# Kernel tuning notes

Measured on AMD Instinct MI355X. Metric: run time of the kernel, lower is better.

Reference implementation:

```python
import jax, jax.numpy as jnp
import numpy as np

T = 2048          # tokens (prefill, single sequence)
H = 4096          # hidden_size
NH = 32           # num attention heads
NKV = 8           # num kv heads (GQA)
HD = H // NH      # head_dim = 128
EPS = 1e-5
THETA = 10000.0


def setup_inputs() -> dict:
    key = jax.random.key(0)
    k0, k1, k2 = jax.random.split(key, 3)
    return {
        "positions": jnp.arange(T, dtype=jnp.int64 if jax.config.jax_enable_x64 else jnp.int32),
        "hidden_states": jax.random.normal(k0, (T, H), dtype=jnp.float32),
        "w_qkv": jax.random.normal(k1, (H, (NH + 2 * NKV) * HD), dtype=jnp.float32) * 0.02,
        "w_o": jax.random.normal(k2, (NH * HD, H), dtype=jnp.float32) * 0.02,
        "q_norm_w": jnp.ones((NH, HD), dtype=jnp.float32),
        "k_norm_w": jnp.ones((NKV, HD), dtype=jnp.float32),
    }


def _layer_norm(x, w, eps):
    # x: [T, n_heads, HD], w: [n_heads, HD]; mean/var over last dim, fp32 math
    xf = x.astype(jnp.float32)
    mean = xf.mean(-1, keepdims=True)
    var = jnp.square(xf - mean).mean(-1, keepdims=True)
    y = (xf - mean) * jax.lax.rsqrt(var + eps)
    return (w.astype(jnp.float32)[None] * y).astype(x.dtype)


def _rope_interleaved(x, positions):
    # non-neox (GPT-J) style: rotate interleaved pairs. x: [T, n, HD]
    inv_freq = 1.0 / (THETA ** (jnp.arange(0, HD, 2, dtype=jnp.float32) / HD))  # [HD/2]
    freqs = positions.astype(jnp.float32)[:, None] * inv_freq[None, :]          # [T, HD/2]
    cos = jnp.cos(freqs)[:, None, :]  # [T,1,HD/2]
    sin = jnp.sin(freqs)[:, None, :]
    x1 = x[..., 0::2]
    x2 = x[..., 1::2]
    o1 = x1 * cos - x2 * sin
    o2 = x2 * cos + x1 * sin
    return jnp.stack([o1, o2], axis=-1).reshape(x.shape)


def reference(positions, hidden_states, w_qkv, w_o, q_norm_w, k_norm_w):
    qkv = hidden_states @ w_qkv  # [T, (NH+2*NKV)*HD]
    q, k, v = jnp.split(qkv, [NH * HD, (NH + NKV) * HD], axis=-1)
    q = q.reshape(T, NH, HD)
    k = k.reshape(T, NKV, HD)
    v = v.reshape(T, NKV, HD)

    # per-head qk LayerNorm
    q = _layer_norm(q, q_norm_w, EPS)
    k = _layer_norm(k, k_norm_w, EPS)

    # non-neox RoPE
    q = _rope_interleaved(q, positions)
    k = _rope_interleaved(k, positions)

    # GQA: expand kv heads to NH
    rep = NH // NKV
    k = jnp.repeat(k, rep, axis=1)  # [T, NH, HD]
    v = jnp.repeat(v, rep, axis=1)

    scale = HD ** -0.5
    scores = jnp.einsum("qhd,khd->hqk", q * scale, k)  # [NH, T, T]
    causal = jnp.tril(jnp.ones((T, T), dtype=bool))
    scores = jnp.where(causal[None], scores, jnp.finfo(scores.dtype).min)
    probs = jax.nn.softmax(scores, axis=-1)
    attn = jnp.einsum("hqk,khd->qhd", probs, v).reshape(T, NH * HD)

    return attn @ w_o  # [T, H]
```

## Files before the change

### kernel.cpp

```cpp
#include <hip/hip_runtime.h>
#include <cstdint>
#include <cstddef>

#define T_SEQ   2048
#define H_DIM   4096
#define NH_Q    32
#define NKV_H   8
#define HD_     128
#define QKV_N   6144
#define EPS_F   1e-5f
#define ATT_SCALE 0.08838834764831845f
#define LN_THETA  9.210340371976184f

typedef __attribute__((ext_vector_type(8))) short bf16x8;
typedef __attribute__((ext_vector_type(4))) float f32x4;

static __device__ __forceinline__ unsigned short f2bf(float f) {
  union { float f; uint32_t u; } v; v.f = f;
  uint32_t u = v.u;
  u += 0x7fff + ((u >> 16) & 1);
  return (unsigned short)(u >> 16);
}
static __device__ __forceinline__ float bf2f(unsigned short h) {
  union { uint32_t u; float f; } v; v.u = ((uint32_t)h) << 16;
  return v.f;
}

static __device__ __forceinline__ void gld_lds16(const void* g, void* l) {
  __builtin_amdgcn_global_load_lds(
      (const __attribute__((address_space(1))) unsigned int*)g,
      (__attribute__((address_space(3))) unsigned int*)l, 16, 0, 0);
}

__global__ void convert_bf16_kernel(const float* __restrict__ in,
                                    unsigned short* __restrict__ out, int n4) {
  int i = blockIdx.x * blockDim.x + threadIdx.x;
  if (i < n4) {
    float4 f = *(const float4*)(in + (size_t)i * 4);
    ushort4 o;
    o.x = f2bf(f.x); o.y = f2bf(f.y); o.z = f2bf(f.z); o.w = f2bf(f.w);
    *(ushort4*)(out + (size_t)i * 4) = o;
  }
}

__global__ void transpose_bf16_kernel(const float* __restrict__ in,
                                      unsigned short* __restrict__ out,
                                      int R, int C) {
  __shared__ float tile[32][33];
  int c0 = blockIdx.x * 32, r0 = blockIdx.y * 32;
  int tx = threadIdx.x, ty = threadIdx.y;
  for (int i = 0; i < 32; i += 8)
    tile[ty + i][tx] = in[(size_t)(r0 + ty + i) * C + c0 + tx];
  __syncthreads();
  for (int i = 0; i < 32; i += 8)
    out[(size_t)(c0 + ty + i) * R + r0 + tx] = f2bf(tile[tx][ty + i]);
}

template <bool BF16OUT>
__global__ __launch_bounds__(512) void gemm256_kernel(
    const unsigned short* __restrict__ A, const unsigned short* __restrict__ Bt,
    void* __restrict__ C0, void* __restrict__ C1,
    int M, int N, int Ks, int Kl) {
  __shared__ unsigned short As[2][256 * 64];
  __shared__ unsigned short Bs[2][256 * 64];
  const int tid = threadIdx.x, lane = tid & 63, wid = tid >> 6;
  const int wm = wid >> 2, wn = wid & 3;
  const int g = lane >> 4, s = lane & 15, s7 = s & 7;
  const int m0 = blockIdx.y * 256, n0 = blockIdx.x * 256;
  const int z = blockIdx.z;
  const unsigned short* Ab = A + (size_t)z * Kl;
  const unsigned short* Bb = Bt + (size_t)z * Kl;
  void* Cp = z ? C1 : C0;
  const int NT = Kl >> 6;

  const int lr = lane >> 3, lc = lane & 7;
  const size_t srcoff = (size_t)lr * Ks + (size_t)((lc ^ lr) * 8);

  auto stage_half = [&](const unsigned short* grow, unsigned short* lhalf) {
    gld_lds16(grow + (size_t)(wid * 16) * Ks + srcoff, lhalf + wid * 1024);
    gld_lds16(grow + (size_t)(wid * 16 + 8) * Ks + srcoff,
              lhalf + wid * 1024 + 512);
  };

  const int aroff = (wm * 128 + s) * 64;
  const int broff = (wn * 64 + s) * 64;
  const int ck0 = ((0 * 4 + g) ^ s7) * 8;
  const int ck1 = ((1 * 4 + g) ^ s7) * 8;

  f32x4 acc[8][4] = {};

  stage_half(Ab + (size_t)(m0)       * Ks, &As[0][0]);
  stage_half(Ab + (size_t)(m0 + 128) * Ks, &As[0][128 * 64]);
  stage_half(Bb + (size_t)(n0)       * Ks, &Bs[0][0]);
  stage_half(Bb + (size_t)(n0 + 128) * Ks, &Bs[0][128 * 64]);
  stage_half(Bb + (size_t)(n0)       * Ks + 64, &Bs[1][0]);
  stage_half(Bb + (size_t)(n0 + 128) * Ks + 64, &Bs[1][128 * 64]);
  asm volatile("s_waitcnt vmcnt(4)" ::: "memory");
  __builtin_amdgcn_s_barrier();

  auto tile_step = [&](unsigned short* cA, unsigned short* cB,
                       unsigned short* nA, int t) {
    const int k0 = t << 6;
    bf16x8 bfr[4][2];
#pragma unroll
    for (int fc = 0; fc < 4; fc++) {
      bfr[fc][0] = *(const bf16x8*)(cB + broff + fc * 1024 + ck0);
      bfr[fc][1] = *(const bf16x8*)(cB + broff + fc * 1024 + ck1);
    }
#pragma unroll
    for (int ph = 0; ph < 4; ph++) {
      bf16x8 a[2][2];
#pragma unroll
      for (int i = 0; i < 2; i++) {
        const int fr = ph * 2 + i;
        a[i][0] = *(const bf16x8*)(cA + aroff + fr * 1024 + ck0);
        a[i][1] = *(const bf16x8*)(cA + aroff + fr * 1024 + ck1);
      }
      if (ph == 0 && t + 1 < NT)
        stage_half(Ab + (size_t)(m0) * Ks + k0 + 64, nA);
      if (ph == 1 && t + 1 < NT)
        stage_half(Ab + (size_t)(m0 + 128) * Ks + k0 + 64, nA + 128 * 64);
      if (ph == 2 && t + 2 < NT)
        stage_half(Bb + (size_t)(n0) * Ks + k0 + 128, cB);
      if (ph == 3 && t + 2 < NT)
        stage_half(Bb + (size_t)(n0 + 128) * Ks + k0 + 128, cB + 128 * 64);
      __builtin_amdgcn_s_barrier();
      __builtin_amdgcn_s_setprio(1);
#pragma unroll
      for (int i = 0; i < 2; i++) {
        const int fr = ph * 2 + i;
#pragma unroll
        for (int fc = 0; fc < 4; fc++)
          acc[fr][fc] = __builtin_amdgcn_mfma_f32_16x16x32_bf16(
              a[i][0], bfr[fc][0], acc[fr][fc], 0, 0, 0);
      }
#pragma unroll
      for (int i = 0; i < 2; i++) {
        const int fr = ph * 2 + i;
#pragma unroll
        for (int fc = 0; fc < 4; fc++)
          acc[fr][fc] = __builtin_amdgcn_mfma_f32_16x16x32_bf16(
              a[i][1], bfr[fc][1], acc[fr][fc], 0, 0, 0);
      }
      __builtin_amdgcn_s_setprio(0);
      if (ph == 3) {
        if (t + 2 < NT) asm volatile("s_waitcnt vmcnt(4)" ::: "memory");
        else            asm volatile("s_waitcnt vmcnt(0)" ::: "memory");
      }
      __builtin_amdgcn_s_barrier();
    }
  };

  for (int t = 0; t < NT; t += 2) {
    tile_step(&As[0][0], &Bs[0][0], &As[1][0], t);
    tile_step(&As[1][0], &Bs[1][0], &As[0][0], t + 1);
  }

#pragma unroll
  for (int fr = 0; fr < 8; fr++)
#pragma unroll
    for (int fc = 0; fc < 4; fc++)
#pragma unroll
      for (int r = 0; r < 4; r++) {
        int m = m0 + wm * 128 + fr * 16 + g * 4 + r;
        int n = n0 + wn * 64 + fc * 16 + s;
        float v = acc[fr][fc][r];
        if (BF16OUT) ((unsigned short*)Cp)[(size_t)m * N + n] = f2bf(v);
        else         ((float*)Cp)[(size_t)m * N + n] = v;
      }
}

__global__ void addf_kernel(float* __restrict__ o, const float* __restrict__ p,
                            int n4) {
  int i = blockIdx.x * blockDim.x + threadIdx.x;
  if (i < n4) {
    float4 a = *(const float4*)(o + (size_t)i * 4);
    float4 b = *(const float4*)(p + (size_t)i * 4);
    a.x += b.x; a.y += b.y; a.z += b.z; a.w += b.w;
    *(float4*)(o + (size_t)i * 4) = a;
  }
}

__global__ __launch_bounds__(256) void ln_rope_kernel(
    unsigned short* __restrict__ qkv, const int* __restrict__ positions,
    const float* __restrict__ qw, const float* __restrict__ kw) {
  const int wid = threadIdx.x >> 6, lane = threadIdx.x & 63;
  const int rid = blockIdx.x * 4 + wid;
  const int t = rid / 40, hh = rid % 40;
  const bool isq = hh < NH_Q;
  const int col = isq ? hh * HD_ : H_DIM + (hh - NH_Q) * HD_;
  unsigned short* row = qkv + (size_t)t * QKV_N + col;

  uint32_t both = *(const uint32_t*)(row + lane * 2);
  float x1 = bf2f((unsigned short)(both & 0xffff));
  float x2 = bf2f((unsigned short)(both >> 16));
  float ssum = x1 + x2, ssq = x1 * x1 + x2 * x2;
  for (int off = 1; off < 64; off <<= 1) {
    ssum += __shfl_xor(ssum, off, 64);
    ssq  += __shfl_xor(ssq,  off, 64);
  }
  float mean = ssum * (1.0f / HD_);
  float var  = ssq * (1.0f / HD_) - mean * mean;
  float rs = rsqrtf(var + EPS_F);
  const float* w = isq ? (qw + hh * HD_) : (kw + (hh - NH_Q) * HD_);
  float2 wv = *(const float2*)(w + lane * 2);
  float y1 = (x1 - mean) * rs * wv.x;
  float y2 = (x2 - mean) * rs * wv.y;
  float pos = (float)positions[t];
  float inv = __expf(-((float)(2 * lane) * (1.0f / HD_)) * LN_THETA);
  float fr = pos * inv;
  float c = cosf(fr), sn = sinf(fr);
  float o1 = y1 * c - y2 * sn;
  float o2 = y2 * c + y1 * sn;
  if (isq) { o1 *= ATT_SCALE; o2 *= ATT_SCALE; }
  *(uint32_t*)(row + lane * 2) =
      (uint32_t)f2bf(o1) | ((uint32_t)f2bf(o2) << 16);
}

__global__ void vt_kernel(const unsigned short* __restrict__ qkv,
                          unsigned short* __restrict__ vt) {
  __shared__ unsigned short tile[32][33];
  const int kvh = blockIdx.z;
  const int t0 = blockIdx.x * 32, d0 = blockIdx.y * 32;
  const int tx = threadIdx.x, ty = threadIdx.y;
  for (int i = 0; i < 32; i += 8)
    tile[ty + i][tx] =
        qkv[(size_t)(t0 + ty + i) * QKV_N + H_DIM + NKV_H * HD_ + kvh * HD_ + d0 + tx];
  __syncthreads();
  for (int i = 0; i < 32; i += 8)
    vt[((size_t)kvh * HD_ + d0 + ty + i) * T_SEQ + t0 + tx] = tile[tx][ty + i];
}

__global__ __launch_bounds__(256) void attn_kernel(
    const unsigned short* __restrict__ qkv, const unsigned short* __restrict__ vt,
    unsigned short* __restrict__ out) {
  __shared__ unsigned short Ks[64 * 136];
  __shared__ unsigned short Vs[128 * 72];
  __shared__ unsigned short Ps[4][16 * 72];
  const int tid = threadIdx.x, lane = tid & 63, wid = tid >> 6;
  const int g = lane >> 4, s = lane & 15;
  const int h = blockIdx.y;
  const int kvh = h >> 2;
  const int NQT = T_SEQ / 64;

  for (int half = 0; half < 2; half++) {
    const int qt = (half == 0) ? (int)blockIdx.x : NQT - 1 - (int)blockIdx.x;
    const int q0 = qt * 64;

    bf16x8 qf[4];
    {
      const unsigned short* qrow =
          qkv + (size_t)(q0 + wid * 16 + s) * QKV_N + h * HD_;
      for (int ks = 0; ks < 4; ks++)
        qf[ks] = *(const bf16x8*)(qrow + ks * 32 + g * 8);
    }
    f32x4 o[8] = {};
    float m_i[4], l_i[4];
    for (int r = 0; r < 4; r++) { m_i[r] = -1e30f; l_i[r] = 0.f; }

    const int ktiles = qt + 1;
    for (int kt = 0; kt < ktiles; kt++) {
      const int k0 = kt * 64;
      __syncthreads();
      {
        int kr = tid >> 4, kc = tid & 15;
        for (int p = 0; p < 4; p++) {
          bf16x8 v = *(const bf16x8*)(qkv + (size_t)(k0 + kr + p * 16) * QKV_N +
                                      H_DIM + kvh * HD_ + kc * 8);
          *(bf16x8*)&Ks[(kr + p * 16) * 136 + kc * 8] = v;
        }
        int vr = tid >> 3, vc = tid & 7;
        for (int p = 0; p < 4; p++) {
          bf16x8 v = *(const bf16x8*)(vt + ((size_t)kvh * HD_ + vr + p * 32) * T_SEQ +
                                      k0 + vc * 8);
          *(bf16x8*)&Vs[(vr + p * 32) * 72 + vc * 8] = v;
        }
      }
      __syncthreads();
      f32x4 sa[4] = {};
      __builtin_amdgcn_s_setprio(1);
      for (int nt = 0; nt < 4; nt++)
        for (int ks = 0; ks < 4; ks++) {
          bf16x8 kb = *(const bf16x8*)&Ks[(nt * 16 + s) * 136 + ks * 32 + g * 8];
          sa[nt] = __builtin_amdgcn_mfma_f32_16x16x32_bf16(qf[ks], kb, sa[nt], 0, 0, 0);
        }
      __builtin_amdgcn_s_setprio(0);
      if (kt == ktiles - 1) {
        for (int nt = 0; nt < 4; nt++)
          for (int r = 0; r < 4; r++)
            if (k0 + nt * 16 + s > q0 + wid * 16 + g * 4 + r) sa[nt][r] = -1e30f;
      }
      float alpha[4];
      for (int r = 0; r < 4; r++) {
        float mx = fmaxf(fmaxf(sa[0][r], sa[1][r]), fmaxf(sa[2][r], sa[3][r]));
        for (int off = 1; off < 16; off <<= 1) mx = fmaxf(mx, __shfl_xor(mx, off, 64));
        float mn = fmaxf(m_i[r], mx);
        alpha[r] = __expf(m_i[r] - mn);
        m_i[r] = mn;
        float rsum = 0.f;
        for (int nt = 0; nt < 4; nt++) {
          float p = __expf(sa[nt][r] - mn);
          sa[nt][r] = p;
          rsum += p;
        }
        for (int off = 1; off < 16; off <<= 1) rsum += __shfl_xor(rsum, off, 64);
        l_i[r] = l_i[r] * alpha[r] + rsum;
      }
      for (int nt = 0; nt < 4; nt++)
        for (int r = 0; r < 4; r++)
          Ps[wid][(g * 4 + r) * 72 + nt * 16 + s] = f2bf(sa[nt][r]);
      for (int ot = 0; ot < 8; ot++)
        for (int r = 0; r < 4; r++) o[ot][r] *= alpha[r];
      __syncthreads();
      __builtin_amdgcn_s_setprio(1);
      for (int ot = 0; ot < 8; ot++)
        for (int ks = 0; ks < 2; ks++) {
          bf16x8 pa = *(const bf16x8*)&Ps[wid][s * 72 + ks * 32 + g * 8];
          bf16x8 vb = *(const bf16x8*)&Vs[(ot * 16 + s) * 72 + ks * 32 + g * 8];
          o[ot] = __builtin_amdgcn_mfma_f32_16x16x32_bf16(pa, vb, o[ot], 0, 0, 0);
        }
      __builtin_amdgcn_s_setprio(0);
    }
    const size_t obase = (size_t)(q0 + wid * 16);
    for (int ot = 0; ot < 8; ot++)
      for (int r = 0; r < 4; r++) {
        float v = o[ot][r] / l_i[r];
        out[(obase + g * 4 + r) * (size_t)(NH_Q * HD_) + h * HD_ + ot * 16 + s] =
            f2bf(v);
      }
  }
}

extern "C" void kernel_launch(void* const* d_in, const int* in_sizes, int n_in,
                              void* d_out, int out_size, void* d_ws, size_t ws_size,
                              hipStream_t stream) {
  const int*   positions = (const int*)d_in[0];
  const float* hs        = (const float*)d_in[1];
  const float* w_qkv     = (const float*)d_in[2];
  const float* w_o       = (const float*)d_in[3];
  const float* q_norm_w  = (const float*)d_in[4];
  const float* k_norm_w  = (const float*)d_in[5];
  float* out = (float*)d_out;

  char* p = (char*)d_ws;
  unsigned short* hsb   = (unsigned short*)p; p += (size_t)T_SEQ * H_DIM * 2;
  unsigned short* wqkvT = (unsigned short*)p; p += (size_t)QKV_N * H_DIM * 2;
  unsigned short* woT   = (unsigned short*)p; p += (size_t)H_DIM * H_DIM * 2;
  unsigned short* qkvb  = (unsigned short*)p; p += (size_t)T_SEQ * QKV_N * 2;
  unsigned short* attnb = (unsigned short*)p; p += (size_t)T_SEQ * H_DIM * 2;
  unsigned short* vtb   = (unsigned short*)p; p += (size_t)NKV_H * HD_ * T_SEQ * 2;
  float* part1 = (float*)wqkvT;

  convert_bf16_kernel<<<(T_SEQ * H_DIM / 4 + 255) / 256, 256, 0, stream>>>(
      hs, hsb, T_SEQ * H_DIM / 4);
  transpose_bf16_kernel<<<dim3(QKV_N / 32, H_DIM / 32), dim3(32, 8), 0, stream>>>(
      w_qkv, wqkvT, H_DIM, QKV_N);
  transpose_bf16_kernel<<<dim3(H_DIM / 32, H_DIM / 32), dim3(32, 8), 0, stream>>>(
      w_o, woT, H_DIM, H_DIM);
  gemm256_kernel<true><<<dim3(QKV_N / 256, T_SEQ / 256, 1), 512, 0, stream>>>(
      hsb, wqkvT, qkvb, nullptr, T_SEQ, QKV_N, H_DIM, H_DIM);
  ln_rope_kernel<<<T_SEQ * (NH_Q + NKV_H) / 4, 256, 0, stream>>>(
      qkvb, positions, q_norm_w, k_norm_w);
  vt_kernel<<<dim3(T_SEQ / 32, HD_ / 32, NKV_H), dim3(32, 8), 0, stream>>>(qkvb, vtb);
  attn_kernel<<<dim3(T_SEQ / 128, NH_Q), 256, 0, stream>>>(qkvb, vtb, attnb);
  gemm256_kernel<false><<<dim3(H_DIM / 256, T_SEQ / 256, 2), 512, 0, stream>>>(
      attnb, woT, out, part1, T_SEQ, H_DIM, H_DIM, H_DIM / 2);
  addf_kernel<<<(T_SEQ * H_DIM / 4 + 255) / 256, 256, 0, stream>>>(
      out, part1, T_SEQ * H_DIM / 4);
}
```

Measured before the change: 571.3 us.

## Simplify GEMM pipeline to whole-tile double buffering with one barrier per K-step

Replaces the staggered per-phase staging (A one tile ahead, B two tiles ahead, with barriers after every phase) with a plain double buffer. The whole next A and B tile is issued at the start of each K-step, followed by a single vmcnt(0) wait and barrier at the end. This cuts the barrier count per K-step from eight to one and simplifies the schedule. In exchange, prefetch depth for B drops from two tiles to one, and the wait drains all loads, so memory latency may be less hidden.

Result: no change. 574.5 us (+0.6%).

```diff
diff --git a/kernel.cpp b/kernel.cpp
--- a/kernel.cpp
+++ b/kernel.cpp
@@ -81,6 +81,13 @@
     gld_lds16(grow + (size_t)(wid * 16 + 8) * Ks + srcoff,
               lhalf + wid * 1024 + 512);
   };
+  auto stage_tile = [&](int t, unsigned short* dA, unsigned short* dB) {
+    const int kk = t << 6;
+    stage_half(Ab + (size_t)(m0)       * Ks + kk, dA);
+    stage_half(Ab + (size_t)(m0 + 128) * Ks + kk, dA + 128 * 64);
+    stage_half(Bb + (size_t)(n0)       * Ks + kk, dB);
+    stage_half(Bb + (size_t)(n0 + 128) * Ks + kk, dB + 128 * 64);
+  };
 
   const int aroff = (wm * 128 + s) * 64;
   const int broff = (wn * 64 + s) * 64;
@@ -89,18 +96,13 @@
 
   f32x4 acc[8][4] = {};
 
-  stage_half(Ab + (size_t)(m0)       * Ks, &As[0][0]);
-  stage_half(Ab + (size_t)(m0 + 128) * Ks, &As[0][128 * 64]);
-  stage_half(Bb + (size_t)(n0)       * Ks, &Bs[0][0]);
-  stage_half(Bb + (size_t)(n0 + 128) * Ks, &Bs[0][128 * 64]);
-  stage_half(Bb + (size_t)(n0)       * Ks + 64, &Bs[1][0]);
-  stage_half(Bb + (size_t)(n0 + 128) * Ks + 64, &Bs[1][128 * 64]);
-  asm volatile("s_waitcnt vmcnt(4)" ::: "memory");
+  stage_tile(0, &As[0][0], &Bs[0][0]);
+  asm volatile("s_waitcnt vmcnt(0)" ::: "memory");
   __builtin_amdgcn_s_barrier();
 
   auto tile_step = [&](unsigned short* cA, unsigned short* cB,
-                       unsigned short* nA, int t) {
-    const int k0 = t << 6;
+                       unsigned short* nA, unsigned short* nB, int t) {
+    if (t + 1 < NT) stage_tile(t + 1, nA, nB);
     bf16x8 bfr[4][2];
 #pragma unroll
     for (int fc = 0; fc < 4; fc++) {
@@ -116,15 +118,6 @@
         a[i][0] = *(const bf16x8*)(cA + aroff + fr * 1024 + ck0);
         a[i][1] = *(const bf16x8*)(cA + aroff + fr * 1024 + ck1);
       }
-      if (ph == 0 && t + 1 < NT)
-        stage_half(Ab + (size_t)(m0) * Ks + k0 + 64, nA);
-      if (ph == 1 && t + 1 < NT)
-        stage_half(Ab + (size_t)(m0 + 128) * Ks + k0 + 64, nA + 128 * 64);
-      if (ph == 2 && t + 2 < NT)
-        stage_half(Bb + (size_t)(n0) * Ks + k0 + 128, cB);
-      if (ph == 3 && t + 2 < NT)
-        stage_half(Bb + (size_t)(n0 + 128) * Ks + k0 + 128, cB + 128 * 64);
-      __builtin_amdgcn_s_barrier();
       __builtin_amdgcn_s_setprio(1);
 #pragma unroll
       for (int i = 0; i < 2; i++) {
@@ -143,17 +136,14 @@
               a[i][1], bfr[fc][1], acc[fr][fc], 0, 0, 0);
       }
       __builtin_amdgcn_s_setprio(0);
-      if (ph == 3) {
-        if (t + 2 < NT) asm volatile("s_waitcnt vmcnt(4)" ::: "memory");
-        else            asm volatile("s_waitcnt vmcnt(0)" ::: "memory");
-      }
-      __builtin_amdgcn_s_barrier();
     }
+    asm volatile("s_waitcnt vmcnt(0)" ::: "memory");
+    __builtin_amdgcn_s_barrier();
   };
 
   for (int t = 0; t < NT; t += 2) {
-    tile_step(&As[0][0], &Bs[0][0], &As[1][0], t);
-    tile_step(&As[1][0], &Bs[1][0], &As[0][0], t + 1);
+    tile_step(&As[0][0], &Bs[0][0], &As[1][0], &Bs[1][0], t);
+    tile_step(&As[1][0], &Bs[1][0], &As[0][0], &Bs[0][0], t + 1);
   }
 
 #pragma unroll
```

## Widen attention query tile to 128 rows and vectorize weight transpose

Applied to the files above, without the earlier changes.

The attention kernel now runs 8 waves per block over 128-query tiles, so each K/V tile staged in LDS is reused by twice as many query rows, with the causal mask applied to the last two key tiles. The weight transpose kernel moves to 64x64 tiles with float4 loads and ushort4 stores to cut memory transactions. The trade-off is fewer attention blocks (256) on the GPU, which may hurt occupancy and load balance, and more LDS and register use per block.

Result: no change. 569.4 us (-0.3%).

```diff
diff --git a/kernel.cpp b/kernel.cpp
--- a/kernel.cpp
+++ b/kernel.cpp
@@ -43,17 +43,28 @@
   }
 }
 
-__global__ void transpose_bf16_kernel(const float* __restrict__ in,
-                                      unsigned short* __restrict__ out,
-                                      int R, int C) {
-  __shared__ float tile[32][33];
-  int c0 = blockIdx.x * 32, r0 = blockIdx.y * 32;
-  int tx = threadIdx.x, ty = threadIdx.y;
-  for (int i = 0; i < 32; i += 8)
-    tile[ty + i][tx] = in[(size_t)(r0 + ty + i) * C + c0 + tx];
+__global__ __launch_bounds__(256) void transpose_bf16_kernel(
+    const float* __restrict__ in, unsigned short* __restrict__ out,
+    int R, int C) {
+  __shared__ float tile[64][65];
+  const int c0 = blockIdx.x * 64, r0 = blockIdx.y * 64;
+  const int tx = threadIdx.x, ty = threadIdx.y;
+  for (int i = 0; i < 64; i += 16) {
+    float4 v = *(const float4*)(in + (size_t)(r0 + ty + i) * C + c0 + tx * 4);
+    tile[ty + i][tx * 4 + 0] = v.x;
+    tile[ty + i][tx * 4 + 1] = v.y;
+    tile[ty + i][tx * 4 + 2] = v.z;
+    tile[ty + i][tx * 4 + 3] = v.w;
+  }
   __syncthreads();
-  for (int i = 0; i < 32; i += 8)
-    out[(size_t)(c0 + ty + i) * R + r0 + tx] = f2bf(tile[tx][ty + i]);
+  for (int i = 0; i < 64; i += 16) {
+    ushort4 o4;
+    o4.x = f2bf(tile[tx * 4 + 0][ty + i]);
+    o4.y = f2bf(tile[tx * 4 + 1][ty + i]);
+    o4.z = f2bf(tile[tx * 4 + 2][ty + i]);
+    o4.w = f2bf(tile[tx * 4 + 3][ty + i]);
+    *(ushort4*)(out + (size_t)(c0 + ty + i) * R + r0 + tx * 4) = o4;
+  }
 }
 
 template <bool BF16OUT>
@@ -231,21 +242,21 @@
     vt[((size_t)kvh * HD_ + d0 + ty + i) * T_SEQ + t0 + tx] = tile[tx][ty + i];
 }
 
-__global__ __launch_bounds__(256) void attn_kernel(
+__global__ __launch_bounds__(512) void attn_kernel(
     const unsigned short* __restrict__ qkv, const unsigned short* __restrict__ vt,
     unsigned short* __restrict__ out) {
   __shared__ unsigned short Ks[64 * 136];
   __shared__ unsigned short Vs[128 * 72];
-  __shared__ unsigned short Ps[4][16 * 72];
+  __shared__ unsigned short Ps[8][16 * 72];
   const int tid = threadIdx.x, lane = tid & 63, wid = tid >> 6;
   const int g = lane >> 4, s = lane & 15;
   const int h = blockIdx.y;
   const int kvh = h >> 2;
-  const int NQT = T_SEQ / 64;
+  const int NQT = T_SEQ / 128;
 
   for (int half = 0; half < 2; half++) {
     const int qt = (half == 0) ? (int)blockIdx.x : NQT - 1 - (int)blockIdx.x;
-    const int q0 = qt * 64;
+    const int q0 = qt * 128;
 
     bf16x8 qf[4];
     {
@@ -258,22 +269,22 @@
     float m_i[4], l_i[4];
     for (int r = 0; r < 4; r++) { m_i[r] = -1e30f; l_i[r] = 0.f; }
 
-    const int ktiles = qt + 1;
+    const int ktiles = 2 * qt + 2;
     for (int kt = 0; kt < ktiles; kt++) {
       const int k0 = kt * 64;
       __syncthreads();
       {
         int kr = tid >> 4, kc = tid & 15;
-        for (int p = 0; p < 4; p++) {
-          bf16x8 v = *(const bf16x8*)(qkv + (size_t)(k0 + kr + p * 16) * QKV_N +
+        for (int p = 0; p < 2; p++) {
+          bf16x8 v = *(const bf16x8*)(qkv + (size_t)(k0 + kr + p * 32) * QKV_N +
                                       H_DIM + kvh * HD_ + kc * 8);
-          *(bf16x8*)&Ks[(kr + p * 16) * 136 + kc * 8] = v;
+          *(bf16x8*)&Ks[(kr + p * 32) * 136 + kc * 8] = v;
         }
         int vr = tid >> 3, vc = tid & 7;
-        for (int p = 0; p < 4; p++) {
-          bf16x8 v = *(const bf16x8*)(vt + ((size_t)kvh * HD_ + vr + p * 32) * T_SEQ +
+        for (int p = 0; p < 2; p++) {
+          bf16x8 v = *(const bf16x8*)(vt + ((size_t)kvh * HD_ + vr + p * 64) * T_SEQ +
                                       k0 + vc * 8);
-          *(bf16x8*)&Vs[(vr + p * 32) * 72 + vc * 8] = v;
+          *(bf16x8*)&Vs[(vr + p * 64) * 72 + vc * 8] = v;
         }
       }
       __syncthreads();
@@ -285,7 +296,7 @@
           sa[nt] = __builtin_amdgcn_mfma_f32_16x16x32_bf16(qf[ks], kb, sa[nt], 0, 0, 0);
         }
       __builtin_amdgcn_s_setprio(0);
-      if (kt == ktiles - 1) {
+      if (kt >= ktiles - 2) {
         for (int nt = 0; nt < 4; nt++)
           for (int r = 0; r < 4; r++)
             if (k0 + nt * 16 + s > q0 + wid * 16 + g * 4 + r) sa[nt][r] = -1e30f;
@@ -353,16 +364,16 @@
 
   convert_bf16_kernel<<<(T_SEQ * H_DIM / 4 + 255) / 256, 256, 0, stream>>>(
       hs, hsb, T_SEQ * H_DIM / 4);
-  transpose_bf16_kernel<<<dim3(QKV_N / 32, H_DIM / 32), dim3(32, 8), 0, stream>>>(
+  transpose_bf16_kernel<<<dim3(QKV_N / 64, H_DIM / 64), dim3(16, 16), 0, stream>>>(
       w_qkv, wqkvT, H_DIM, QKV_N);
-  transpose_bf16_kernel<<<dim3(H_DIM / 32, H_DIM / 32), dim3(32, 8), 0, stream>>>(
+  transpose_bf16_kernel<<<dim3(H_DIM / 64, H_DIM / 64), dim3(16, 16), 0, stream>>>(
       w_o, woT, H_DIM, H_DIM);
   gemm256_kernel<true><<<dim3(QKV_N / 256, T_SEQ / 256, 1), 512, 0, stream>>>(
       hsb, wqkvT, qkvb, nullptr, T_SEQ, QKV_N, H_DIM, H_DIM);
   ln_rope_kernel<<<T_SEQ * (NH_Q + NKV_H) / 4, 256, 0, stream>>>(
       qkvb, positions, q_norm_w, k_norm_w);
   vt_kernel<<<dim3(T_SEQ / 32, HD_ / 32, NKV_H), dim3(32, 8), 0, stream>>>(qkvb, vtb);
-  attn_kernel<<<dim3(T_SEQ / 128, NH_Q), 256, 0, stream>>>(qkvb, vtb, attnb);
+  attn_kernel<<<dim3(T_SEQ / 256, NH_Q), 512, 0, stream>>>(qkvb, vtb, attnb);
   gemm256_kernel<false><<<dim3(H_DIM / 256, T_SEQ / 256, 2), 512, 0, stream>>>(
       attnb, woT, out, part1, T_SEQ, H_DIM, H_DIM, H_DIM / 2);
   addf_kernel<<<(T_SEQ * H_DIM / 4 + 255) / 256, 256, 0, stream>>>(
```
